# Kernel optimization log

Measured on AMD Instinct MI355X. Metric: run time of the kernel, lower is better.

The kernel has to match this reference:

```python
import jax, jax.numpy as jnp
import numpy as np

N, E, IN_F, G, LATENT, HIDDEN, STEPS = 50000, 800000, 7, 16, 64, 128, 3
LN_EPS = 1e-6  # flax LayerNorm default


def setup_inputs() -> dict:
    key = jax.random.key(0)

    def rn(i, shape, scale=1.0):
        return jax.random.normal(jax.random.fold_in(key, i), shape, dtype=jnp.float32) * scale

    return {
        "nodes": rn(0, (N, IN_F)),
        "senders": jax.random.randint(jax.random.fold_in(key, 1), (E,), 0, N, dtype=jnp.int32),
        "receivers": jax.random.randint(jax.random.fold_in(key, 2), (E,), 0, N, dtype=jnp.int32),
        "g": rn(3, (G,)),
        "embed_w": rn(4, (IN_F, LATENT), IN_F ** -0.5),
        "embed_b": jnp.zeros((LATENT,), jnp.float32),
        "edge_w1_first": rn(5, (2 * LATENT + G, HIDDEN), (2 * LATENT + G) ** -0.5),
        "edge_w1_rest": rn(6, (STEPS - 1, 3 * LATENT + G, HIDDEN), (3 * LATENT + G) ** -0.5),
        "edge_b1": jnp.zeros((STEPS, HIDDEN), jnp.float32),
        "edge_w2": rn(7, (STEPS, HIDDEN, LATENT), HIDDEN ** -0.5),
        "edge_b2": jnp.zeros((STEPS, LATENT), jnp.float32),
        "node_w1": rn(8, (STEPS, 2 * LATENT + G, HIDDEN), (2 * LATENT + G) ** -0.5),
        "node_b1": jnp.zeros((STEPS, HIDDEN), jnp.float32),
        "node_w2": rn(9, (STEPS, HIDDEN, LATENT), HIDDEN ** -0.5),
        "node_b2": jnp.zeros((STEPS, LATENT), jnp.float32),
        "ln_scale": jnp.ones((STEPS, LATENT), jnp.float32),
        "ln_bias": jnp.zeros((STEPS, LATENT), jnp.float32),
        "dec_w": rn(10, (LATENT, IN_F), LATENT ** -0.5),
        "dec_b": jnp.zeros((IN_F,), jnp.float32),
    }


def _layer_norm(x, scale, bias):
    mu = jnp.mean(x, axis=-1, keepdims=True)
    var = jnp.var(x, axis=-1, keepdims=True)
    return (x - mu) * jax.lax.rsqrt(var + LN_EPS) * scale + bias


def reference(nodes, senders, receivers, g, embed_w, embed_b,
              edge_w1_first, edge_w1_rest, edge_b1, edge_w2, edge_b2,
              node_w1, node_b1, node_w2, node_b2, ln_scale, ln_bias,
              dec_w, dec_b):
    n_node = nodes.shape[0]
    n_edge = senders.shape[0]
    # node embedder (GraphMapFeatures with Dense(latent_size))
    h = nodes @ embed_w + embed_b                      # [N, LATENT]
    ge = jnp.broadcast_to(g[None, :], (n_edge, g.shape[0]))  # globals per edge
    gn = jnp.broadcast_to(g[None, :], (n_node, g.shape[0]))  # globals per node
    e = None
    for t in range(STEPS):
        s = h[senders]                                 # [E, LATENT] gather
        r = h[receivers]                               # [E, LATENT] gather
        if t == 0:
            # edges are None on the first step -> concat(senders, receivers, globals)
            e_in = jnp.concatenate([s, r, ge], axis=1)
            w1 = edge_w1_first
        else:
            e_in = jnp.concatenate([e, s, r, ge], axis=1)
            w1 = edge_w1_rest[t - 1]
        # edge MLP: Dense(hidden)+gelu, Dense(latent)
        e = jax.nn.gelu(e_in @ w1 + edge_b1[t]) @ edge_w2[t] + edge_b2[t]
        # aggregate messages at receivers (jraph default segment_sum)
        recv = jax.ops.segment_sum(e, receivers, num_segments=n_node)
        # node MLP on concat(nodes, received, globals)
        n_in = jnp.concatenate([h, recv, gn], axis=1)
        upd = jax.nn.gelu(n_in @ node_w1[t] + node_b1[t]) @ node_w2[t] + node_b2[t]
        h = h + upd                                    # skip connection on nodes
        h = _layer_norm(h, ln_scale[t], ln_bias[t])
    # node decoder back to in_features
    return h @ dec_w + dec_b
```

## Files before the change

### kernel.cpp

```cpp
#include <hip/hip_runtime.h>

#define NN 50000
#define NE 800000
#define INF 7
#define GD 16
#define LAT 64
#define HID 128

typedef unsigned short u16;
typedef __attribute__((ext_vector_type(8))) __bf16 bf16x8;
typedef __attribute__((ext_vector_type(4))) float f32x4;

__device__ __forceinline__ float bf2f(u16 u) {
  union { unsigned int i; float f; } v; v.i = ((unsigned int)u) << 16; return v.f;
}
__device__ __forceinline__ u16 f2bf(float f) {
  union { float f; unsigned int i; } v; v.f = f;
  unsigned int x = v.i;
  return (u16)((x + 0x7fffu + ((x >> 16) & 1u)) >> 16);
}
__device__ __forceinline__ float gelu(float x) {
  float u = x * x;
  float p = fmaf(0.044715f * u, x, x);
  float e = __expf(-1.5957691216057308f * p);
  return x * __builtin_amdgcn_rcpf(e + 1.0f);
}

struct PackJobs {
  const float* src[13];
  u16* dst[13];
  int K[13];
  int N[13];
  int KC[13];
};

__global__ void pack_all(PackJobs J) {
  const int j = blockIdx.y;
  const int KC = J.KC[j];
  const float* W = J.src[j];
  u16* out = J.dst[j];
  int t = blockIdx.x * blockDim.x + threadIdx.x;
  if (KC == 0) {
    if (t < 32) out[t] = (t < GD) ? f2bf(W[t]) : (u16)0;
    return;
  }
  const int K = J.K[j], N = J.N[j];
  const int NT = N >> 4;
  if (t >= KC * NT * 64) return;
  int l = t & 63;
  int nt = (t >> 6) % NT;
  int kc = t / (64 * NT);
  int n = nt * 16 + (l & 15);
  int kbase = kc * 32 + (l >> 4) * 8;
  ushort4 lo, hi;
  u16 v[8];
#pragma unroll
  for (int jj = 0; jj < 8; ++jj) {
    int k = kbase + jj;
    v[jj] = (k < K) ? f2bf(W[k * N + n]) : (u16)0;
  }
  lo.x = v[0]; lo.y = v[1]; lo.z = v[2]; lo.w = v[3];
  hi.x = v[4]; hi.y = v[5]; hi.z = v[6]; hi.w = v[7];
  ushort4* dst = (ushort4*)&out[(size_t)t * 8];
  dst[0] = lo; dst[1] = hi;
}

__global__ void embed_kernel(const float* __restrict__ nodes, const float* __restrict__ w,
                             const float* __restrict__ b, float* __restrict__ h,
                             u16* __restrict__ hbf) {
  int gid = blockIdx.x * blockDim.x + threadIdx.x;
  if (gid >= NN * LAT) return;
  int n = gid >> 6, j = gid & 63;
  float acc = b[j];
#pragma unroll
  for (int k = 0; k < INF; ++k)
    acc = fmaf(nodes[n * INF + k], w[k * LAT + j], acc);
  h[gid] = acc;
  hbf[gid] = f2bf(acc);
}

template <int KC, bool FIRST>
__launch_bounds__(256)
__global__ void edge_mfma(const u16* __restrict__ hbf, u16* __restrict__ ebuf,
                          float* __restrict__ recvbuf,
                          const int* __restrict__ snd, const int* __restrict__ rcv,
                          const u16* __restrict__ gpad,
                          const u16* __restrict__ w1p, const float* __restrict__ b1,
                          const u16* __restrict__ w2p, const float* __restrict__ b2) {
  __shared__ __align__(16) u16 hid[32 * 136];
  __shared__ __align__(16) u16 easm[32 * 64];
  __shared__ int rcvs[32];

  const int tid = threadIdx.x;
  const int lane = tid & 63;
  const int w = tid >> 6;
  const int l15 = lane & 15;
  const int q = lane >> 4;
  const int mr = w & 1;
  const int ntb1 = (w >> 1) * 4;
  const int ntb2 = (w >> 1) * 2;
  const int arow = mr * 16 + l15;
  const int NTILE = NE / 32;

  float bb1[4], bb2[2];
#pragma unroll
  for (int i = 0; i < 4; ++i) bb1[i] = b1[(ntb1 + i) * 16 + l15];
#pragma unroll
  for (int i = 0; i < 2; ++i) bb2[i] = b2[(ntb2 + i) * 16 + l15];

  int s_cur = 0, r_cur = 0;
  if (blockIdx.x < NTILE) {
    const int eg0 = blockIdx.x * 32 + arow;
    s_cur = snd[eg0];
    r_cur = rcv[eg0];
  }

  for (int tile = blockIdx.x; tile < NTILE; tile += gridDim.x) {
    const int ebase = tile * 32;
    const int eg = ebase + arow;
    const int soff = s_cur * 64;
    const int roff = r_cur * 64;
    if (tid < 32) rcvs[tid] = rcv[ebase + tid];

    {
      int tn = tile + gridDim.x;
      if (tn < NTILE) {
        const int egn = tn * 32 + arow;
        s_cur = snd[egn];
        r_cur = rcv[egn];
      }
    }

    {
      f32x4 acc[4];
#pragma unroll
      for (int i = 0; i < 4; ++i) acc[i] = (f32x4){bb1[i], bb1[i], bb1[i], bb1[i]};
#pragma unroll
      for (int kc = 0; kc < KC; ++kc) {
        const u16* abase;
        if (FIRST) {
          abase = (kc < 2) ? &hbf[soff + kc * 32]
                : (kc < 4) ? &hbf[roff + (kc - 2) * 32]
                :            &gpad[0];
        } else {
          abase = (kc < 2) ? &ebuf[(size_t)eg * 64 + kc * 32]
                : (kc < 4) ? &hbf[soff + (kc - 2) * 32]
                : (kc < 6) ? &hbf[roff + (kc - 4) * 32]
                :            &gpad[0];
        }
        bf16x8 a = *(const bf16x8*)&abase[q * 8];
#pragma unroll
        for (int i = 0; i < 4; ++i) {
          bf16x8 b = *(const bf16x8*)&w1p[(size_t)((kc * 8 + ntb1 + i) * 64 + lane) * 8];
          acc[i] = __builtin_amdgcn_mfma_f32_16x16x32_bf16(a, b, acc[i], 0, 0, 0);
        }
      }
#pragma unroll
      for (int i = 0; i < 4; ++i) {
        const int col = (ntb1 + i) * 16 + l15;
#pragma unroll
        for (int r4 = 0; r4 < 4; ++r4) {
          const int row = mr * 16 + q * 4 + r4;
          hid[row * 136 + col] = f2bf(gelu(acc[i][r4]));
        }
      }
    }
    __syncthreads();
    {
      f32x4 acc[2];
#pragma unroll
      for (int i = 0; i < 2; ++i) acc[i] = (f32x4){bb2[i], bb2[i], bb2[i], bb2[i]};
#pragma unroll
      for (int kc = 0; kc < 4; ++kc) {
        bf16x8 a = *(const bf16x8*)&hid[arow * 136 + kc * 32 + q * 8];
#pragma unroll
        for (int i = 0; i < 2; ++i) {
          bf16x8 b = *(const bf16x8*)&w2p[(size_t)((kc * 4 + ntb2 + i) * 64 + lane) * 8];
          acc[i] = __builtin_amdgcn_mfma_f32_16x16x32_bf16(a, b, acc[i], 0, 0, 0);
        }
      }
#pragma unroll
      for (int i = 0; i < 2; ++i) {
        const int col = (ntb2 + i) * 16 + l15;
#pragma unroll
        for (int r4 = 0; r4 < 4; ++r4) {
          const int row = mr * 16 + q * 4 + r4;
          const float v = acc[i][r4];
          easm[row * 64 + col] = f2bf(v);
          atomicAdd(&recvbuf[(size_t)rcvs[row] * 64 + col], v);
        }
      }
    }
    __syncthreads();
    ((uint4*)&ebuf[(size_t)ebase * 64])[tid] = ((const uint4*)easm)[tid];
  }
}

__launch_bounds__(256)
__global__ void node_mfma(float* __restrict__ h, u16* __restrict__ hbf,
                          const float* __restrict__ recvb,
                          const u16* __restrict__ gpad,
                          const u16* __restrict__ w1p, const float* __restrict__ b1,
                          const u16* __restrict__ w2p, const float* __restrict__ b2,
                          const float* __restrict__ lns, const float* __restrict__ lnb) {
  __shared__ __align__(16) u16 hid[32 * 136];
  __shared__ __align__(16) float outs[32 * 68];

  const int tid = threadIdx.x;
  const int lane = tid & 63;
  const int w = tid >> 6;
  const int l15 = lane & 15;
  const int q = lane >> 4;
  const int mr = w & 1;
  const int ntb1 = (w >> 1) * 4;
  const int ntb2 = (w >> 1) * 2;
  const int arow = mr * 16 + l15;

  float bb1[4], bb2[2];
#pragma unroll
  for (int i = 0; i < 4; ++i) bb1[i] = b1[(ntb1 + i) * 16 + l15];
#pragma unroll
  for (int i = 0; i < 2; ++i) bb2[i] = b2[(ntb2 + i) * 16 + l15];

  const int nrow = tid >> 3;
  const int jc = (tid & 7) * 8;
  float sc8[8], bi8[8];
#pragma unroll
  for (int k = 0; k < 8; ++k) { sc8[k] = lns[jc + k]; bi8[k] = lnb[jc + k]; }

  const int NT = (NN + 31) / 32;
  for (int tile = blockIdx.x; tile < NT; tile += gridDim.x) {
    const int nbase = tile * 32;
    const int na = min(nbase + arow, NN - 1) * 64;

    {
      f32x4 acc[4];
#pragma unroll
      for (int i = 0; i < 4; ++i) acc[i] = (f32x4){bb1[i], bb1[i], bb1[i], bb1[i]};
#pragma unroll
      for (int kc = 0; kc < 5; ++kc) {
        bf16x8 a;
        if (kc < 2) {
          a = *(const bf16x8*)&hbf[na + kc * 32 + q * 8];
        } else if (kc < 4) {
          const float* rp = &recvb[na + (kc - 2) * 32 + q * 8];
          union { u16 u[8]; bf16x8 v; } cv;
#pragma unroll
          for (int jj = 0; jj < 8; ++jj) cv.u[jj] = f2bf(rp[jj]);
          a = cv.v;
        } else {
          a = *(const bf16x8*)&gpad[q * 8];
        }
#pragma unroll
        for (int i = 0; i < 4; ++i) {
          bf16x8 b = *(const bf16x8*)&w1p[(size_t)((kc * 8 + ntb1 + i) * 64 + lane) * 8];
          acc[i] = __builtin_amdgcn_mfma_f32_16x16x32_bf16(a, b, acc[i], 0, 0, 0);
        }
      }
#pragma unroll
      for (int i = 0; i < 4; ++i) {
        const int col = (ntb1 + i) * 16 + l15;
#pragma unroll
        for (int r4 = 0; r4 < 4; ++r4) {
          const int row = mr * 16 + q * 4 + r4;
          hid[row * 136 + col] = f2bf(gelu(acc[i][r4]));
        }
      }
    }
    __syncthreads();
    {
      f32x4 acc[2];
#pragma unroll
      for (int i = 0; i < 2; ++i) acc[i] = (f32x4){bb2[i], bb2[i], bb2[i], bb2[i]};
#pragma unroll
      for (int kc = 0; kc < 4; ++kc) {
        bf16x8 a = *(const bf16x8*)&hid[arow * 136 + kc * 32 + q * 8];
#pragma unroll
        for (int i = 0; i < 2; ++i) {
          bf16x8 b = *(const bf16x8*)&w2p[(size_t)((kc * 4 + ntb2 + i) * 64 + lane) * 8];
          acc[i] = __builtin_amdgcn_mfma_f32_16x16x32_bf16(a, b, acc[i], 0, 0, 0);
        }
      }
#pragma unroll
      for (int i = 0; i < 2; ++i) {
        const int col = (ntb2 + i) * 16 + l15;
#pragma unroll
        for (int r4 = 0; r4 < 4; ++r4) {
          const int row = mr * 16 + q * 4 + r4;
          outs[row * 68 + col] = acc[i][r4];
        }
      }
    }
    __syncthreads();
    {
      const int n = nbase + nrow;
      if (n < NN) {
        float x[8];
        float4 hv0 = *(const float4*)&h[n * 64 + jc];
        float4 hv1 = *(const float4*)&h[n * 64 + jc + 4];
        x[0] = hv0.x + outs[nrow * 68 + jc + 0];
        x[1] = hv0.y + outs[nrow * 68 + jc + 1];
        x[2] = hv0.z + outs[nrow * 68 + jc + 2];
        x[3] = hv0.w + outs[nrow * 68 + jc + 3];
        x[4] = hv1.x + outs[nrow * 68 + jc + 4];
        x[5] = hv1.y + outs[nrow * 68 + jc + 5];
        x[6] = hv1.z + outs[nrow * 68 + jc + 6];
        x[7] = hv1.w + outs[nrow * 68 + jc + 7];
        float s = 0.f, qq = 0.f;
#pragma unroll
        for (int k = 0; k < 8; ++k) { s += x[k]; qq += x[k] * x[k]; }
#pragma unroll
        for (int off = 1; off < 8; off <<= 1) {
          s += __shfl_xor(s, off);
          qq += __shfl_xor(qq, off);
        }
        float mean = s * (1.0f / 64.0f);
        float var = fmaxf(qq * (1.0f / 64.0f) - mean * mean, 0.0f);
        float rstd = rsqrtf(var + 1e-6f);
        float o[8];
        ushort4 ob0, ob1;
#pragma unroll
        for (int k = 0; k < 8; ++k) o[k] = (x[k] - mean) * rstd * sc8[k] + bi8[k];
        *(float4*)&h[n * 64 + jc]     = make_float4(o[0], o[1], o[2], o[3]);
        *(float4*)&h[n * 64 + jc + 4] = make_float4(o[4], o[5], o[6], o[7]);
        ob0.x = f2bf(o[0]); ob0.y = f2bf(o[1]); ob0.z = f2bf(o[2]); ob0.w = f2bf(o[3]);
        ob1.x = f2bf(o[4]); ob1.y = f2bf(o[5]); ob1.z = f2bf(o[6]); ob1.w = f2bf(o[7]);
        *(ushort4*)&hbf[n * 64 + jc]     = ob0;
        *(ushort4*)&hbf[n * 64 + jc + 4] = ob1;
      }
    }
    __syncthreads();
  }
}

__global__ void decode_kernel(const float* __restrict__ h, const float* __restrict__ w,
                              const float* __restrict__ b, float* __restrict__ out) {
  int gid = blockIdx.x * blockDim.x + threadIdx.x;
  if (gid >= NN * INF) return;
  int n = gid / 7, f = gid % 7;
  float acc = b[f];
#pragma unroll
  for (int k = 0; k < LAT; ++k)
    acc = fmaf(h[n * 64 + k], w[k * 7 + f], acc);
  out[gid] = acc;
}

extern "C" void kernel_launch(void* const* d_in, const int* in_sizes, int n_in,
                              void* d_out, int out_size, void* d_ws, size_t ws_size,
                              hipStream_t stream) {
  const float* nodes = (const float*)d_in[0];
  const int* senders = (const int*)d_in[1];
  const int* recvrs  = (const int*)d_in[2];
  const float* g     = (const float*)d_in[3];
  const float* emb_w = (const float*)d_in[4];
  const float* emb_b = (const float*)d_in[5];
  const float* ew1f  = (const float*)d_in[6];
  const float* ew1r  = (const float*)d_in[7];
  const float* eb1   = (const float*)d_in[8];
  const float* ew2   = (const float*)d_in[9];
  const float* eb2   = (const float*)d_in[10];
  const float* nw1   = (const float*)d_in[11];
  const float* nb1   = (const float*)d_in[12];
  const float* nw2   = (const float*)d_in[13];
  const float* nb2   = (const float*)d_in[14];
  const float* lns   = (const float*)d_in[15];
  const float* lnb   = (const float*)d_in[16];
  const float* dw    = (const float*)d_in[17];
  const float* db    = (const float*)d_in[18];

  char* cur = (char*)d_ws;
  float* h      = (float*)cur;  cur += (size_t)NN * LAT * 4;
  float* recvb  = (float*)cur;  cur += (size_t)NN * LAT * 4;
  u16*   ebuf   = (u16*)cur;    cur += (size_t)NE * LAT * 2;
  u16*   hbf    = (u16*)cur;    cur += (size_t)NN * LAT * 2;
  u16*   ew1p[3]; for (int t = 0; t < 3; ++t) { ew1p[t] = (u16*)cur; cur += 7 * 8 * 64 * 8 * 2; }
  u16*   ew2p[3]; for (int t = 0; t < 3; ++t) { ew2p[t] = (u16*)cur; cur += 4 * 4 * 64 * 8 * 2; }
  u16*   nw1p[3]; for (int t = 0; t < 3; ++t) { nw1p[t] = (u16*)cur; cur += 5 * 8 * 64 * 8 * 2; }
  u16*   nw2p[3]; for (int t = 0; t < 3; ++t) { nw2p[t] = (u16*)cur; cur += 4 * 4 * 64 * 8 * 2; }
  u16*   gpad   = (u16*)cur;    cur += 64;

  PackJobs J;
  J.src[0] = ew1f;                       J.dst[0] = ew1p[0]; J.K[0] = 144; J.N[0] = 128; J.KC[0] = 5;
  J.src[1] = ew1r;                       J.dst[1] = ew1p[1]; J.K[1] = 208; J.N[1] = 128; J.KC[1] = 7;
  J.src[2] = ew1r + (size_t)208 * 128;   J.dst[2] = ew1p[2]; J.K[2] = 208; J.N[2] = 128; J.KC[2] = 7;
  for (int t = 0; t < 3; ++t) {
    J.src[3 + t] = ew2 + (size_t)t * 128 * 64;  J.dst[3 + t] = ew2p[t]; J.K[3 + t] = 128; J.N[3 + t] = 64; J.KC[3 + t] = 4;
    J.src[6 + t] = nw1 + (size_t)t * 144 * 128; J.dst[6 + t] = nw1p[t]; J.K[6 + t] = 144; J.N[6 + t] = 128; J.KC[6 + t] = 5;
    J.src[9 + t] = nw2 + (size_t)t * 128 * 64;  J.dst[9 + t] = nw2p[t]; J.K[9 + t] = 128; J.N[9 + t] = 64; J.KC[9 + t] = 4;
  }
  J.src[12] = g; J.dst[12] = gpad; J.K[12] = 0; J.N[12] = 0; J.KC[12] = 0;
  pack_all<<<dim3(16, 13), 256, 0, stream>>>(J);

  embed_kernel<<<(NN * LAT + 255) / 256, 256, 0, stream>>>(nodes, emb_w, emb_b, h, hbf);

  for (int t = 0; t < 3; ++t) {
    hipMemsetAsync(recvb, 0, (size_t)NN * LAT * 4, stream);
    if (t == 0)
      edge_mfma<5, true><<<2048, 256, 0, stream>>>(hbf, ebuf, recvb,
          senders, recvrs, gpad, ew1p[0], eb1, ew2p[0], eb2);
    else
      edge_mfma<7, false><<<2048, 256, 0, stream>>>(hbf, ebuf, recvb,
          senders, recvrs, gpad, ew1p[t], eb1 + t * 128, ew2p[t], eb2 + t * 64);
    node_mfma<<<1563, 256, 0, stream>>>(h, hbf, recvb, gpad,
        nw1p[t], nb1 + t * 128, nw2p[t], nb2 + t * 64,
        lns + t * 64, lnb + t * 64);
  }

  decode_kernel<<<(NN * INF + 255) / 256, 256, 0, stream>>>(h, dw, db, (float*)d_out);
}
```

Baseline: 750.8 us.

## Sort edges by receiver and coalesce segment-sum atomics within each lane

Adds a counting sort of edges by receiver (histogram, three-pass scan, atomic scatter) run once per call. The edge kernel then reads sender and receiver indices from the sorted arrays. Each lane merges consecutive rows that share a receiver before issuing atomicAdd, which cuts atomic traffic and improves locality of receiver gathers. This costs several extra small kernels, and the per-edge state is now stored in sorted order, which is consistent across steps because every step uses the same sorted arrays.

```diff
diff --git a/kernel.cpp b/kernel.cpp
--- a/kernel.cpp
+++ b/kernel.cpp
@@ -6,6 +6,7 @@
 #define GD 16
 #define LAT 64
 #define HID 128
+#define NB 196
 
 typedef unsigned short u16;
 typedef __attribute__((ext_vector_type(8))) __bf16 bf16x8;
@@ -65,6 +66,57 @@
   dst[0] = lo; dst[1] = hi;
 }
 
+__global__ void hist_kernel(const int* __restrict__ rcv, int* __restrict__ cnt) {
+  int e = blockIdx.x * blockDim.x + threadIdx.x;
+  if (e < NE) atomicAdd(&cnt[rcv[e]], 1);
+}
+
+__global__ void scan1(const int* __restrict__ cnt, int* __restrict__ part) {
+  __shared__ int sdata[256];
+  int i = blockIdx.x * 256 + threadIdx.x;
+  sdata[threadIdx.x] = (i < NN) ? cnt[i] : 0;
+  __syncthreads();
+  for (int off = 128; off > 0; off >>= 1) {
+    if (threadIdx.x < off) sdata[threadIdx.x] += sdata[threadIdx.x + off];
+    __syncthreads();
+  }
+  if (threadIdx.x == 0) part[blockIdx.x] = sdata[0];
+}
+
+__global__ void scan2(int* __restrict__ part) {
+  if (threadIdx.x == 0) {
+    int acc = 0;
+    for (int b = 0; b < NB; ++b) { int v = part[b]; part[b] = acc; acc += v; }
+  }
+}
+
+__global__ void scan3(const int* __restrict__ cnt, const int* __restrict__ part,
+                      int* __restrict__ cursor) {
+  __shared__ int sdata[256];
+  int i = blockIdx.x * 256 + threadIdx.x;
+  int v = (i < NN) ? cnt[i] : 0;
+  sdata[threadIdx.x] = v;
+  __syncthreads();
+  for (int off = 1; off < 256; off <<= 1) {
+    int t = (threadIdx.x >= off) ? sdata[threadIdx.x - off] : 0;
+    __syncthreads();
+    sdata[threadIdx.x] += t;
+    __syncthreads();
+  }
+  if (i < NN) cursor[i] = sdata[threadIdx.x] - v + part[blockIdx.x];
+}
+
+__global__ void scatter_kernel(const int* __restrict__ snd, const int* __restrict__ rcv,
+                               int* __restrict__ cursor,
+                               int* __restrict__ ssorted, int* __restrict__ rsorted) {
+  int e = blockIdx.x * blockDim.x + threadIdx.x;
+  if (e >= NE) return;
+  int r = rcv[e];
+  int pos = atomicAdd(&cursor[r], 1);
+  ssorted[pos] = snd[e];
+  rsorted[pos] = r;
+}
+
 __global__ void embed_kernel(const float* __restrict__ nodes, const float* __restrict__ w,
                              const float* __restrict__ b, float* __restrict__ h,
                              u16* __restrict__ hbf) {
@@ -83,7 +135,7 @@
 __launch_bounds__(256)
 __global__ void edge_mfma(const u16* __restrict__ hbf, u16* __restrict__ ebuf,
                           float* __restrict__ recvbuf,
-                          const int* __restrict__ snd, const int* __restrict__ rcv,
+                          const int* __restrict__ ssorted, const int* __restrict__ rsorted,
                           const u16* __restrict__ gpad,
                           const u16* __restrict__ w1p, const float* __restrict__ b1,
                           const u16* __restrict__ w2p, const float* __restrict__ b2) {
@@ -111,8 +163,8 @@
   int s_cur = 0, r_cur = 0;
   if (blockIdx.x < NTILE) {
     const int eg0 = blockIdx.x * 32 + arow;
-    s_cur = snd[eg0];
-    r_cur = rcv[eg0];
+    s_cur = ssorted[eg0];
+    r_cur = rsorted[eg0];
   }
 
   for (int tile = blockIdx.x; tile < NTILE; tile += gridDim.x) {
@@ -120,14 +172,14 @@
     const int eg = ebase + arow;
     const int soff = s_cur * 64;
     const int roff = r_cur * 64;
-    if (tid < 32) rcvs[tid] = rcv[ebase + tid];
+    if (tid < 32) rcvs[tid] = rsorted[ebase + tid];
 
     {
       int tn = tile + gridDim.x;
       if (tn < NTILE) {
         const int egn = tn * 32 + arow;
-        s_cur = snd[egn];
-        r_cur = rcv[egn];
+        s_cur = ssorted[egn];
+        r_cur = rsorted[egn];
       }
     }
 
@@ -179,16 +231,27 @@
           acc[i] = __builtin_amdgcn_mfma_f32_16x16x32_bf16(a, b, acc[i], 0, 0, 0);
         }
       }
+      const int row0 = mr * 16 + q * 4;
 #pragma unroll
       for (int i = 0; i < 2; ++i) {
         const int col = (ntb2 + i) * 16 + l15;
-#pragma unroll
-        for (int r4 = 0; r4 < 4; ++r4) {
-          const int row = mr * 16 + q * 4 + r4;
+        easm[row0 * 64 + col] = f2bf(acc[i][0]);
+        int rp = rcvs[row0];
+        float sum = acc[i][0];
+#pragma unroll
+        for (int r4 = 1; r4 < 4; ++r4) {
+          const int row = row0 + r4;
           const float v = acc[i][r4];
           easm[row * 64 + col] = f2bf(v);
-          atomicAdd(&recvbuf[(size_t)rcvs[row] * 64 + col], v);
-        }
+          const int rr = rcvs[row];
+          if (rr == rp) {
+            sum += v;
+          } else {
+            atomicAdd(&recvbuf[(size_t)rp * 64 + col], sum);
+            rp = rr; sum = v;
+          }
+        }
+        atomicAdd(&recvbuf[(size_t)rp * 64 + col], sum);
       }
     }
     __syncthreads();
@@ -369,15 +432,20 @@
   const float* db    = (const float*)d_in[18];
 
   char* cur = (char*)d_ws;
-  float* h      = (float*)cur;  cur += (size_t)NN * LAT * 4;
-  float* recvb  = (float*)cur;  cur += (size_t)NN * LAT * 4;
-  u16*   ebuf   = (u16*)cur;    cur += (size_t)NE * LAT * 2;
-  u16*   hbf    = (u16*)cur;    cur += (size_t)NN * LAT * 2;
+  float* h       = (float*)cur;  cur += (size_t)NN * LAT * 4;
+  float* recvb   = (float*)cur;  cur += (size_t)NN * LAT * 4;
+  u16*   ebuf    = (u16*)cur;    cur += (size_t)NE * LAT * 2;
+  u16*   hbf     = (u16*)cur;    cur += (size_t)NN * LAT * 2;
+  int*   ssorted = (int*)cur;    cur += (size_t)NE * 4;
+  int*   rsorted = (int*)cur;    cur += (size_t)NE * 4;
+  int*   cnt     = (int*)cur;    cur += (size_t)NN * 4;
+  int*   cursor  = (int*)cur;    cur += (size_t)NN * 4;
+  int*   part    = (int*)cur;    cur += 256 * 4;
   u16*   ew1p[3]; for (int t = 0; t < 3; ++t) { ew1p[t] = (u16*)cur; cur += 7 * 8 * 64 * 8 * 2; }
   u16*   ew2p[3]; for (int t = 0; t < 3; ++t) { ew2p[t] = (u16*)cur; cur += 4 * 4 * 64 * 8 * 2; }
   u16*   nw1p[3]; for (int t = 0; t < 3; ++t) { nw1p[t] = (u16*)cur; cur += 5 * 8 * 64 * 8 * 2; }
   u16*   nw2p[3]; for (int t = 0; t < 3; ++t) { nw2p[t] = (u16*)cur; cur += 4 * 4 * 64 * 8 * 2; }
-  u16*   gpad   = (u16*)cur;    cur += 64;
+  u16*   gpad    = (u16*)cur;    cur += 64;
 
   PackJobs J;
   J.src[0] = ew1f;                       J.dst[0] = ew1p[0]; J.K[0] = 144; J.N[0] = 128; J.KC[0] = 5;
@@ -391,16 +459,23 @@
   J.src[12] = g; J.dst[12] = gpad; J.K[12] = 0; J.N[12] = 0; J.KC[12] = 0;
   pack_all<<<dim3(16, 13), 256, 0, stream>>>(J);
 
+  hipMemsetAsync(cnt, 0, (size_t)NN * 4, stream);
+  hist_kernel<<<(NE + 255) / 256, 256, 0, stream>>>(recvrs, cnt);
+  scan1<<<NB, 256, 0, stream>>>(cnt, part);
+  scan2<<<1, 64, 0, stream>>>(part);
+  scan3<<<NB, 256, 0, stream>>>(cnt, part, cursor);
+  scatter_kernel<<<(NE + 255) / 256, 256, 0, stream>>>(senders, recvrs, cursor, ssorted, rsorted);
+
   embed_kernel<<<(NN * LAT + 255) / 256, 256, 0, stream>>>(nodes, emb_w, emb_b, h, hbf);
 
   for (int t = 0; t < 3; ++t) {
     hipMemsetAsync(recvb, 0, (size_t)NN * LAT * 4, stream);
     if (t == 0)
       edge_mfma<5, true><<<2048, 256, 0, stream>>>(hbf, ebuf, recvb,
-          senders, recvrs, gpad, ew1p[0], eb1, ew2p[0], eb2);
+          ssorted, rsorted, gpad, ew1p[0], eb1, ew2p[0], eb2);
     else
       edge_mfma<7, false><<<2048, 256, 0, stream>>>(hbf, ebuf, recvb,
-          senders, recvrs, gpad, ew1p[t], eb1 + t * 128, ew2p[t], eb2 + t * 64);
+          ssorted, rsorted, gpad, ew1p[t], eb1 + t * 128, ew2p[t], eb2 + t * 64);
     node_mfma<<<1563, 256, 0, stream>>>(h, hbf, recvb, gpad,
         nw1p[t], nb1 + t * 128, nw2p[t], nb2 + t * 64,
         lns + t * 64, lnb + t * 64);
```

Result: slower. 872.1 us (+16.2%).

## Software-pipeline edge MLP with double-buffered LDS, one barrier per tile

Applied to the files above, without the earlier changes.

Restructures the edge kernel's persistent tile loop so that layer 2 (plus the atomics) for the current tile and layer 1 for the next tile run in the same phase, using double-buffered hidden, output and receiver-index shared arrays. This cuts the loop to one __syncthreads per tile instead of two and lets the gather loads of the next tile overlap with atomics and MFMA work from the current one. The cost is double the LDS footprint, which may lower occupancy. It also adds a prologue and epilogue, and the edge write-back is deferred by one iteration.

```diff
diff --git a/kernel.cpp b/kernel.cpp
--- a/kernel.cpp
+++ b/kernel.cpp
@@ -87,9 +87,9 @@
                           const u16* __restrict__ gpad,
                           const u16* __restrict__ w1p, const float* __restrict__ b1,
                           const u16* __restrict__ w2p, const float* __restrict__ b2) {
-  __shared__ __align__(16) u16 hid[32 * 136];
-  __shared__ __align__(16) u16 easm[32 * 64];
-  __shared__ int rcvs[32];
+  __shared__ __align__(16) u16 hid[2][32 * 136];
+  __shared__ __align__(16) u16 easm[2][32 * 64];
+  __shared__ int rcvs[2][32];
 
   const int tid = threadIdx.x;
   const int lane = tid & 63;
@@ -101,6 +101,7 @@
   const int ntb2 = (w >> 1) * 2;
   const int arow = mr * 16 + l15;
   const int NTILE = NE / 32;
+  const int G = gridDim.x;
 
   float bb1[4], bb2[2];
 #pragma unroll
@@ -108,30 +109,92 @@
 #pragma unroll
   for (int i = 0; i < 2; ++i) bb2[i] = b2[(ntb2 + i) * 16 + l15];
 
-  int s_cur = 0, r_cur = 0;
-  if (blockIdx.x < NTILE) {
-    const int eg0 = blockIdx.x * 32 + arow;
-    s_cur = snd[eg0];
-    r_cur = rcv[eg0];
-  }
-
-  for (int tile = blockIdx.x; tile < NTILE; tile += gridDim.x) {
-    const int ebase = tile * 32;
-    const int eg = ebase + arow;
+  int tile = blockIdx.x;
+  int s_cur = snd[tile * 32 + arow];
+  int r_cur = rcv[tile * 32 + arow];
+  int s_nxt = 0, r_nxt = 0;
+  if (tile + G < NTILE) {
+    s_nxt = snd[(tile + G) * 32 + arow];
+    r_nxt = rcv[(tile + G) * 32 + arow];
+  }
+  if (tid < 32) rcvs[0][tid] = rcv[tile * 32 + tid];
+
+  {
+    const int eg = tile * 32 + arow;
     const int soff = s_cur * 64;
     const int roff = r_cur * 64;
-    if (tid < 32) rcvs[tid] = rcv[ebase + tid];
+    f32x4 acc[4];
+#pragma unroll
+    for (int i = 0; i < 4; ++i) acc[i] = (f32x4){bb1[i], bb1[i], bb1[i], bb1[i]};
+#pragma unroll
+    for (int kc = 0; kc < KC; ++kc) {
+      const u16* abase;
+      if (FIRST) {
+        abase = (kc < 2) ? &hbf[soff + kc * 32]
+              : (kc < 4) ? &hbf[roff + (kc - 2) * 32]
+              :            &gpad[0];
+      } else {
+        abase = (kc < 2) ? &ebuf[(size_t)eg * 64 + kc * 32]
+              : (kc < 4) ? &hbf[soff + (kc - 2) * 32]
+              : (kc < 6) ? &hbf[roff + (kc - 4) * 32]
+              :            &gpad[0];
+      }
+      bf16x8 a = *(const bf16x8*)&abase[q * 8];
+#pragma unroll
+      for (int i = 0; i < 4; ++i) {
+        bf16x8 b = *(const bf16x8*)&w1p[(size_t)((kc * 8 + ntb1 + i) * 64 + lane) * 8];
+        acc[i] = __builtin_amdgcn_mfma_f32_16x16x32_bf16(a, b, acc[i], 0, 0, 0);
+      }
+    }
+#pragma unroll
+    for (int i = 0; i < 4; ++i) {
+      const int col = (ntb1 + i) * 16 + l15;
+#pragma unroll
+      for (int r4 = 0; r4 < 4; ++r4) {
+        const int row = mr * 16 + q * 4 + r4;
+        hid[0][row * 136 + col] = f2bf(gelu(acc[i][r4]));
+      }
+    }
+  }
+  __syncthreads();
+
+  int cur = 0;
+  for (; tile < NTILE; tile += G) {
+    const int tnext = tile + G;
+    if (tile != (int)blockIdx.x)
+      ((uint4*)&ebuf[(size_t)(tile - G) * 2048])[tid] = ((const uint4*)easm[cur ^ 1])[tid];
 
     {
-      int tn = tile + gridDim.x;
-      if (tn < NTILE) {
-        const int egn = tn * 32 + arow;
-        s_cur = snd[egn];
-        r_cur = rcv[egn];
-      }
-    }
-
-    {
+      f32x4 acc[2];
+#pragma unroll
+      for (int i = 0; i < 2; ++i) acc[i] = (f32x4){bb2[i], bb2[i], bb2[i], bb2[i]};
+#pragma unroll
+      for (int kc = 0; kc < 4; ++kc) {
+        bf16x8 a = *(const bf16x8*)&hid[cur][arow * 136 + kc * 32 + q * 8];
+#pragma unroll
+        for (int i = 0; i < 2; ++i) {
+          bf16x8 b = *(const bf16x8*)&w2p[(size_t)((kc * 4 + ntb2 + i) * 64 + lane) * 8];
+          acc[i] = __builtin_amdgcn_mfma_f32_16x16x32_bf16(a, b, acc[i], 0, 0, 0);
+        }
+      }
+#pragma unroll
+      for (int i = 0; i < 2; ++i) {
+        const int col = (ntb2 + i) * 16 + l15;
+#pragma unroll
+        for (int r4 = 0; r4 < 4; ++r4) {
+          const int row = mr * 16 + q * 4 + r4;
+          const float v = acc[i][r4];
+          easm[cur][row * 64 + col] = f2bf(v);
+          atomicAdd(&recvbuf[(size_t)rcvs[cur][row] * 64 + col], v);
+        }
+      }
+    }
+
+    if (tnext < NTILE) {
+      if (tid < 32) rcvs[cur ^ 1][tid] = rcv[tnext * 32 + tid];
+      const int egn = tnext * 32 + arow;
+      const int soff = s_nxt * 64;
+      const int roff = r_nxt * 64;
       f32x4 acc[4];
 #pragma unroll
       for (int i = 0; i < 4; ++i) acc[i] = (f32x4){bb1[i], bb1[i], bb1[i], bb1[i]};
@@ -143,7 +206,7 @@
                 : (kc < 4) ? &hbf[roff + (kc - 2) * 32]
                 :            &gpad[0];
         } else {
-          abase = (kc < 2) ? &ebuf[(size_t)eg * 64 + kc * 32]
+          abase = (kc < 2) ? &ebuf[(size_t)egn * 64 + kc * 32]
                 : (kc < 4) ? &hbf[soff + (kc - 2) * 32]
                 : (kc < 6) ? &hbf[roff + (kc - 4) * 32]
                 :            &gpad[0];
@@ -161,39 +224,19 @@
 #pragma unroll
         for (int r4 = 0; r4 < 4; ++r4) {
           const int row = mr * 16 + q * 4 + r4;
-          hid[row * 136 + col] = f2bf(gelu(acc[i][r4]));
-        }
+          hid[cur ^ 1][row * 136 + col] = f2bf(gelu(acc[i][r4]));
+        }
+      }
+      const int t2 = tnext + G;
+      if (t2 < NTILE) {
+        s_nxt = snd[t2 * 32 + arow];
+        r_nxt = rcv[t2 * 32 + arow];
       }
     }
     __syncthreads();
-    {
-      f32x4 acc[2];
-#pragma unroll
-      for (int i = 0; i < 2; ++i) acc[i] = (f32x4){bb2[i], bb2[i], bb2[i], bb2[i]};
-#pragma unroll
-      for (int kc = 0; kc < 4; ++kc) {
-        bf16x8 a = *(const bf16x8*)&hid[arow * 136 + kc * 32 + q * 8];
-#pragma unroll
-        for (int i = 0; i < 2; ++i) {
-          bf16x8 b = *(const bf16x8*)&w2p[(size_t)((kc * 4 + ntb2 + i) * 64 + lane) * 8];
-          acc[i] = __builtin_amdgcn_mfma_f32_16x16x32_bf16(a, b, acc[i], 0, 0, 0);
-        }
-      }
-#pragma unroll
-      for (int i = 0; i < 2; ++i) {
-        const int col = (ntb2 + i) * 16 + l15;
-#pragma unroll
-        for (int r4 = 0; r4 < 4; ++r4) {
-          const int row = mr * 16 + q * 4 + r4;
-          const float v = acc[i][r4];
-          easm[row * 64 + col] = f2bf(v);
-          atomicAdd(&recvbuf[(size_t)rcvs[row] * 64 + col], v);
-        }
-      }
-    }
-    __syncthreads();
-    ((uint4*)&ebuf[(size_t)ebase * 64])[tid] = ((const uint4*)easm)[tid];
-  }
+    cur ^= 1;
+  }
+  ((uint4*)&ebuf[(size_t)(tile - G) * 2048])[tid] = ((const uint4*)easm[cur ^ 1])[tid];
 }
 
 __launch_bounds__(256)
```

Result: slower. 913.4 us (+21.7%).
